# Optimization experiments

Measured on AMD Instinct MI355X. Metric: run time of the kernel, lower is better.

The kernel has to match this reference:

```python
import jax, jax.numpy as jnp
import numpy as np

EPS = 1e-10
NUM_NODES = 100000
OUT_CH = 128
NUM_EDGES = 600000


def setup_inputs() -> dict:
    key = jax.random.key(0)
    k1, k2, k3, k4, k5, k6 = jax.random.split(key, 6)
    emb = jax.random.normal(k1, (NUM_NODES, OUT_CH), dtype=jnp.float32) * 0.02
    edge_index = jax.random.randint(k2, (2, NUM_EDGES), 0, NUM_NODES, dtype=jnp.int32)
    edge_norm = jax.random.uniform(k3, (NUM_EDGES,), dtype=jnp.float32)
    lim = 1.0 / np.sqrt(OUT_CH)
    loc_w = jax.random.uniform(k4, (OUT_CH, OUT_CH), minval=-lim, maxval=lim, dtype=jnp.float32)
    loc_b = jnp.zeros((OUT_CH,), dtype=jnp.float32)
    std_w = jax.random.uniform(k5, (OUT_CH, OUT_CH), minval=-lim, maxval=lim, dtype=jnp.float32)
    std_b = jnp.zeros((OUT_CH,), dtype=jnp.float32)
    return {"emb": emb, "loc_w": loc_w, "loc_b": loc_b, "std_w": std_w,
            "std_b": std_b, "edge_index": edge_index, "edge_norm": edge_norm}


def reference(emb, loc_w, loc_b, std_w, std_b, edge_index, edge_norm):
    sidx, tidx = edge_index[0], edge_index[1]
    # gather-scale-scatter graph conv: message[e] = emb[sidx[e]] * enorm[e]
    message = emb[sidx] * edge_norm[:, None]          # [E, C]
    ptr = jax.ops.segment_sum(message, tidx, num_segments=emb.shape[0])  # [N, C]
    loc = ptr @ loc_w.T + loc_b                        # [N, C]
    std = jax.nn.softplus(ptr @ std_w.T + std_b) + EPS # [N, C]
    # eval mode: emb_out = loc (dist is Normal(loc, std), returned as params)
    return (loc, std)
```

## Files before the change

### kernel.cpp

```cpp
#include <hip/hip_runtime.h>
#include <hip/hip_bf16.h>
#include <stdint.h>

#define OUT_CH 128
#define EPSV 1e-10f

typedef __attribute__((ext_vector_type(4))) float f32x4;
typedef __attribute__((ext_vector_type(8))) short bf16x8;

__device__ __forceinline__ ushort f2bf(float f) {
    union { float f; unsigned u; } a; a.f = f;
    unsigned u = a.u;
    unsigned r = (u + 0x7fffu + ((u >> 16) & 1u)) >> 16;
    return (ushort)r;
}

__device__ __forceinline__ float bflo(unsigned u) { return __uint_as_float(u << 16); }
__device__ __forceinline__ float bfhi(unsigned u) { return __uint_as_float(u & 0xffff0000u); }

__global__ __launch_bounds__(256) void hist_convert_kernel(
    const int* __restrict__ eidx, int* __restrict__ cnt, int E, int HB, int EB,
    const float* __restrict__ locw, const float* __restrict__ stdw,
    int4* __restrict__ Wb, const float* __restrict__ emb, int4* __restrict__ embb4)
{
    int b = blockIdx.x;
    if (b < HB) {
        int e = b * 256 + threadIdx.x;
        if (e < E) atomicAdd(&cnt[eidx[E + e]], 1);
    } else if (b < HB + 16) {
        int q = (b - HB) * 256 + threadIdx.x;
        int r = q >> 4;
        int c = q & 15;
        const float* src = (r < 128) ? (locw + r * 128 + c * 8)
                                     : (stdw + (r - 128) * 128 + c * 8);
        float4 u0 = *reinterpret_cast<const float4*>(src);
        float4 u1 = *reinterpret_cast<const float4*>(src + 4);
        unsigned p0 = (unsigned)f2bf(u0.x) | ((unsigned)f2bf(u0.y) << 16);
        unsigned p1 = (unsigned)f2bf(u0.z) | ((unsigned)f2bf(u0.w) << 16);
        unsigned p2 = (unsigned)f2bf(u1.x) | ((unsigned)f2bf(u1.y) << 16);
        unsigned p3 = (unsigned)f2bf(u1.z) | ((unsigned)f2bf(u1.w) << 16);
        Wb[q] = make_int4((int)p0, (int)p1, (int)p2, (int)p3);
    } else {
        int idx8 = (b - HB - 16) * 256 + threadIdx.x;
        const float4* e4 = (const float4*)emb;
        float4 u0 = e4[(size_t)idx8 * 2];
        float4 u1 = e4[(size_t)idx8 * 2 + 1];
        unsigned p0 = (unsigned)f2bf(u0.x) | ((unsigned)f2bf(u0.y) << 16);
        unsigned p1 = (unsigned)f2bf(u0.z) | ((unsigned)f2bf(u0.w) << 16);
        unsigned p2 = (unsigned)f2bf(u1.x) | ((unsigned)f2bf(u1.y) << 16);
        unsigned p3 = (unsigned)f2bf(u1.z) | ((unsigned)f2bf(u1.w) << 16);
        embb4[idx8] = make_int4((int)p0, (int)p1, (int)p2, (int)p3);
    }
}

__device__ __forceinline__ int block_exscan256(int v, int* lds, int* totalOut) {
    int t = threadIdx.x;
    lds[t] = v; __syncthreads();
    #pragma unroll
    for (int d = 1; d < 256; d <<= 1) {
        int x = (t >= d) ? lds[t - d] : 0;
        __syncthreads();
        lds[t] += x;
        __syncthreads();
    }
    int inc = lds[t];
    int tot = lds[255];
    __syncthreads();
    *totalOut = tot;
    return inc - v;
}

__global__ __launch_bounds__(256) void block_sum_kernel(
    const int* __restrict__ cnt, int* __restrict__ bsum, int N)
{
    __shared__ int lds[256];
    int base = blockIdx.x * 1024;
    int local = 0;
    #pragma unroll
    for (int k = 0; k < 4; ++k) {
        int idx = base + threadIdx.x * 4 + k;
        local += (idx < N) ? cnt[idx] : 0;
    }
    lds[threadIdx.x] = local; __syncthreads();
    for (int d = 128; d > 0; d >>= 1) {
        if (threadIdx.x < d) lds[threadIdx.x] += lds[threadIdx.x + d];
        __syncthreads();
    }
    if (threadIdx.x == 0) bsum[blockIdx.x] = lds[0];
}

__global__ __launch_bounds__(256) void top_scan_kernel(
    const int* __restrict__ bsum, int* __restrict__ bofs, int NB)
{
    __shared__ int lds[256];
    int t = threadIdx.x;
    int v = (t < NB) ? bsum[t] : 0;
    int total;
    int ex = block_exscan256(v, lds, &total);
    if (t < NB) bofs[t] = ex;
}

__global__ __launch_bounds__(256) void scan_final_kernel(
    const int* __restrict__ cnt, const int* __restrict__ bofs,
    int* __restrict__ cursor, int N)
{
    __shared__ int lds[256];
    int base = blockIdx.x * 1024;
    int c[4]; int local = 0;
    #pragma unroll
    for (int k = 0; k < 4; ++k) {
        int idx = base + threadIdx.x * 4 + k;
        c[k] = (idx < N) ? cnt[idx] : 0;
        local += c[k];
    }
    int total;
    int ex = block_exscan256(local, lds, &total);
    int run = bofs[blockIdx.x] + ex;
    #pragma unroll
    for (int k = 0; k < 4; ++k) {
        int idx = base + threadIdx.x * 4 + k;
        if (idx < N) { cursor[idx] = run; run += c[k]; }
    }
}

__global__ __launch_bounds__(256) void fill_kernel(
    const int* __restrict__ eidx, const float* __restrict__ enorm,
    int* __restrict__ cursor, int2* __restrict__ srcw, int E)
{
    int e = blockIdx.x * 256 + threadIdx.x;
    if (e >= E) return;
    int t = eidx[E + e];
    int s = eidx[e];
    float w = enorm[e];
    int pos = atomicAdd(&cursor[t], 1);
    srcw[pos] = make_int2(s, __float_as_int(w));
}

__global__ __launch_bounds__(256) void gather_kernel(
    const uint4* __restrict__ embb4, const int* __restrict__ cursor,
    const int* __restrict__ cnt, const int2* __restrict__ srcw,
    uint4* __restrict__ ptrb4, int N)
{
    int q = (blockIdx.x * 256 + threadIdx.x) >> 4;
    if (q >= N) return;
    int l16 = threadIdx.x & 15;
    int c = cnt[q];
    int o = cursor[q] - c;
    float a0 = 0.f, a1 = 0.f, a2 = 0.f, a3 = 0.f;
    float a4 = 0.f, a5 = 0.f, a6 = 0.f, a7 = 0.f;
    int j = 0;
    for (; j + 2 <= c; j += 2) {
        int2 p0 = srcw[o + j + 0];
        int2 p1 = srcw[o + j + 1];
        uint4 v0 = embb4[(size_t)p0.x * 16 + l16];
        uint4 v1 = embb4[(size_t)p1.x * 16 + l16];
        float w0 = __int_as_float(p0.y), w1 = __int_as_float(p1.y);
        a0 += bflo(v0.x) * w0 + bflo(v1.x) * w1;
        a1 += bfhi(v0.x) * w0 + bfhi(v1.x) * w1;
        a2 += bflo(v0.y) * w0 + bflo(v1.y) * w1;
        a3 += bfhi(v0.y) * w0 + bfhi(v1.y) * w1;
        a4 += bflo(v0.z) * w0 + bflo(v1.z) * w1;
        a5 += bfhi(v0.z) * w0 + bfhi(v1.z) * w1;
        a6 += bflo(v0.w) * w0 + bflo(v1.w) * w1;
        a7 += bfhi(v0.w) * w0 + bfhi(v1.w) * w1;
    }
    if (j < c) {
        int2 p = srcw[o + j];
        uint4 v = embb4[(size_t)p.x * 16 + l16];
        float w = __int_as_float(p.y);
        a0 += bflo(v.x) * w;  a1 += bfhi(v.x) * w;
        a2 += bflo(v.y) * w;  a3 += bfhi(v.y) * w;
        a4 += bflo(v.z) * w;  a5 += bfhi(v.z) * w;
        a6 += bflo(v.w) * w;  a7 += bfhi(v.w) * w;
    }
    uint4 r;
    r.x = (unsigned)f2bf(a0) | ((unsigned)f2bf(a1) << 16);
    r.y = (unsigned)f2bf(a2) | ((unsigned)f2bf(a3) << 16);
    r.z = (unsigned)f2bf(a4) | ((unsigned)f2bf(a5) << 16);
    r.w = (unsigned)f2bf(a6) | ((unsigned)f2bf(a7) << 16);
    ptrb4[(size_t)q * 32 + l16] = r;
}

__global__ __launch_bounds__(256, 4) void gemm_kernel(
    const int4* __restrict__ Wb, const float* __restrict__ locb,
    const float* __restrict__ stdb, float* __restrict__ out, int N)
{
    __shared__ ushort Wt[128 * 128];
    const int t = threadIdx.x;
    const int wave = t >> 6;
    const int lane = t & 63;
    const int grp = lane >> 4;
    const int l16 = lane & 15;
    const int base = blockIdx.x * 128 + wave * 32;

    const ushort* ptrb = (const ushort*)out;
    int r0 = base + l16;      if (r0 > N - 1) r0 = N - 1;
    int r1 = base + 16 + l16; if (r1 > N - 1) r1 = N - 1;

    bf16x8 a0[4], a1[4];
    #pragma unroll
    for (int s = 0; s < 4; ++s) {
        a0[s] = *reinterpret_cast<const bf16x8*>(ptrb + (size_t)r0 * 256 + s * 32 + grp * 8);
        a1[s] = *reinterpret_cast<const bf16x8*>(ptrb + (size_t)r1 * 256 + s * 32 + grp * 8);
    }

    #pragma unroll
    for (int h = 0; h < 2; ++h) {
        if (h) __syncthreads();
        #pragma unroll
        for (int i = 0; i < 8; ++i) {
            int q = i * 256 + t;
            int r = q >> 4;
            int c = q & 15;
            *reinterpret_cast<int4*>(&Wt[r * 128 + ((c ^ (r & 15)) << 3)]) =
                Wb[(h * 128 + r) * 16 + c];
        }
        __syncthreads();

        f32x4 acc0[8], acc1[8];
        #pragma unroll
        for (int j = 0; j < 8; ++j) {
            acc0[j] = (f32x4){0.f, 0.f, 0.f, 0.f};
            acc1[j] = (f32x4){0.f, 0.f, 0.f, 0.f};
        }

        #pragma unroll
        for (int j = 0; j < 8; ++j) {
            int cb = (j * 16 + l16) * 128;
            #pragma unroll
            for (int s = 0; s < 4; ++s) {
                int c = s * 4 + grp;
                bf16x8 bfr = *reinterpret_cast<const bf16x8*>(&Wt[cb + ((c ^ l16) << 3)]);
                acc0[j] = __builtin_amdgcn_mfma_f32_16x16x32_bf16(a0[s], bfr, acc0[j], 0, 0, 0);
                acc1[j] = __builtin_amdgcn_mfma_f32_16x16x32_bf16(a1[s], bfr, acc1[j], 0, 0, 0);
            }
        }

        float* dst = h ? (out + (size_t)N * OUT_CH) : out;
        #pragma unroll
        for (int j = 0; j < 8; ++j) {
            int col = j * 16 + l16;
            float bias = h ? stdb[col] : locb[col];
            #pragma unroll
            for (int tile = 0; tile < 2; ++tile) {
                #pragma unroll
                for (int rg = 0; rg < 4; ++rg) {
                    int node = base + tile * 16 + grp * 4 + rg;
                    if (node < N) {
                        float x = (tile ? acc1[j][rg] : acc0[j][rg]) + bias;
                        if (h) x = __logf(1.0f + __expf(x)) + EPSV;
                        dst[(size_t)node * OUT_CH + col] = x;
                    }
                }
            }
        }
    }
}

extern "C" void kernel_launch(void* const* d_in, const int* in_sizes, int n_in,
                              void* d_out, int out_size, void* d_ws, size_t ws_size,
                              hipStream_t stream) {
    const float* emb  = (const float*)d_in[0];
    const float* locw = (const float*)d_in[1];
    const float* locb = (const float*)d_in[2];
    const float* stdw = (const float*)d_in[3];
    const float* stdb = (const float*)d_in[4];
    const int*   eidx = (const int*)d_in[5];
    const float* enorm= (const float*)d_in[6];
    float* out = (float*)d_out;

    const int N = in_sizes[0] / OUT_CH;
    const int E = in_sizes[6];
    const int NB = (N + 1023) / 1024;
    const int HB = (E + 255) / 256;
    const int EB = (N * (OUT_CH / 8) + 255) / 256;

    int* cnt    = (int*)d_ws;
    int* cursor = cnt + N;
    int* bsum   = cursor + N;
    int* bofs   = bsum + 256;
    int2* srcw  = (int2*)(((uintptr_t)(bofs + 256) + 255) & ~(uintptr_t)255);
    int4* Wb    = (int4*)(((uintptr_t)(srcw + E) + 255) & ~(uintptr_t)255);

    unsigned* embb = (unsigned*)(out + (size_t)N * OUT_CH);

    hipMemsetAsync(cnt, 0, (size_t)N * sizeof(int), stream);

    hist_convert_kernel<<<HB + 16 + EB, 256, 0, stream>>>(
        eidx, cnt, E, HB, EB, locw, stdw, Wb, emb, (int4*)embb);
    block_sum_kernel<<<NB, 256, 0, stream>>>(cnt, bsum, N);
    top_scan_kernel<<<1, 256, 0, stream>>>(bsum, bofs, NB);
    scan_final_kernel<<<NB, 256, 0, stream>>>(cnt, bofs, cursor, N);
    fill_kernel<<<(E + 255) / 256, 256, 0, stream>>>(eidx, enorm, cursor, srcw, E);

    uint4* ptrb4 = (uint4*)out;
    long gthreads = (long)N * 16;
    gather_kernel<<<(int)((gthreads + 255) / 256), 256, 0, stream>>>(
        (const uint4*)embb, cursor, cnt, srcw, ptrb4, N);

    int nblocks = (N + 127) / 128;
    gemm_kernel<<<nblocks, 256, 0, stream>>>(Wb, locb, stdb, out, N);
}
```

Measured before the change: 279.8 us.

## Pair two nodes per thread group in gather; read GEMM weights directly from global

The gather kernel now has each 16-lane group accumulate two destination nodes (q and q+N/2) in an interleaved loop, giving more independent loads in flight per thread at the cost of more registers and divergence when degrees differ. The GEMM drops the LDS weight staging and __syncthreads. Each wave computes 16 rows across all 256 output columns, loading B fragments directly from the global bf16 weight buffer, which is assumed to stay in cache. This removes the LDS fill and barriers but makes every wave fetch the full weight matrix.

```diff
diff --git a/kernel.cpp b/kernel.cpp
--- a/kernel.cpp
+++ b/kernel.cpp
@@ -139,119 +139,166 @@
 __global__ __launch_bounds__(256) void gather_kernel(
     const uint4* __restrict__ embb4, const int* __restrict__ cursor,
     const int* __restrict__ cnt, const int2* __restrict__ srcw,
-    uint4* __restrict__ ptrb4, int N)
-{
-    int q = (blockIdx.x * 256 + threadIdx.x) >> 4;
-    if (q >= N) return;
-    int l16 = threadIdx.x & 15;
-    int c = cnt[q];
-    int o = cursor[q] - c;
-    float a0 = 0.f, a1 = 0.f, a2 = 0.f, a3 = 0.f;
-    float a4 = 0.f, a5 = 0.f, a6 = 0.f, a7 = 0.f;
+    uint4* __restrict__ ptrb4, int N, int Nh)
+{
+    int idx = blockIdx.x * 256 + threadIdx.x;
+    int qa = idx >> 4;
+    if (qa >= Nh) return;
+    int l16 = idx & 15;
+    int qb = qa + Nh;
+    bool hasB = qb < N;
+
+    int ca = cnt[qa];
+    int oa = cursor[qa] - ca;
+    int cb = 0, ob = 0;
+    if (hasB) { cb = cnt[qb]; ob = cursor[qb] - cb; }
+
+    float a0=0.f,a1=0.f,a2=0.f,a3=0.f,a4=0.f,a5=0.f,a6=0.f,a7=0.f;
+    float b0=0.f,b1=0.f,b2=0.f,b3=0.f,b4=0.f,b5=0.f,b6=0.f,b7=0.f;
+
+    int m = ca < cb ? ca : cb;
     int j = 0;
-    for (; j + 2 <= c; j += 2) {
-        int2 p0 = srcw[o + j + 0];
-        int2 p1 = srcw[o + j + 1];
+    for (; j + 2 <= m; j += 2) {
+        int2 pa0 = srcw[oa + j];
+        int2 pa1 = srcw[oa + j + 1];
+        int2 pb0 = srcw[ob + j];
+        int2 pb1 = srcw[ob + j + 1];
+        uint4 va0 = embb4[(size_t)pa0.x * 16 + l16];
+        uint4 va1 = embb4[(size_t)pa1.x * 16 + l16];
+        uint4 vb0 = embb4[(size_t)pb0.x * 16 + l16];
+        uint4 vb1 = embb4[(size_t)pb1.x * 16 + l16];
+        float wa0 = __int_as_float(pa0.y), wa1 = __int_as_float(pa1.y);
+        float wb0 = __int_as_float(pb0.y), wb1 = __int_as_float(pb1.y);
+        a0 += bflo(va0.x)*wa0 + bflo(va1.x)*wa1;  a1 += bfhi(va0.x)*wa0 + bfhi(va1.x)*wa1;
+        a2 += bflo(va0.y)*wa0 + bflo(va1.y)*wa1;  a3 += bfhi(va0.y)*wa0 + bfhi(va1.y)*wa1;
+        a4 += bflo(va0.z)*wa0 + bflo(va1.z)*wa1;  a5 += bfhi(va0.z)*wa0 + bfhi(va1.z)*wa1;
+        a6 += bflo(va0.w)*wa0 + bflo(va1.w)*wa1;  a7 += bfhi(va0.w)*wa0 + bfhi(va1.w)*wa1;
+        b0 += bflo(vb0.x)*wb0 + bflo(vb1.x)*wb1;  b1 += bfhi(vb0.x)*wb0 + bfhi(vb1.x)*wb1;
+        b2 += bflo(vb0.y)*wb0 + bflo(vb1.y)*wb1;  b3 += bfhi(vb0.y)*wb0 + bfhi(vb1.y)*wb1;
+        b4 += bflo(vb0.z)*wb0 + bflo(vb1.z)*wb1;  b5 += bfhi(vb0.z)*wb0 + bfhi(vb1.z)*wb1;
+        b6 += bflo(vb0.w)*wb0 + bflo(vb1.w)*wb1;  b7 += bfhi(vb0.w)*wb0 + bfhi(vb1.w)*wb1;
+    }
+    for (; j < m; ++j) {
+        int2 pa = srcw[oa + j];
+        int2 pb = srcw[ob + j];
+        uint4 va = embb4[(size_t)pa.x * 16 + l16];
+        uint4 vb = embb4[(size_t)pb.x * 16 + l16];
+        float wa = __int_as_float(pa.y), wb = __int_as_float(pb.y);
+        a0 += bflo(va.x)*wa;  a1 += bfhi(va.x)*wa;
+        a2 += bflo(va.y)*wa;  a3 += bfhi(va.y)*wa;
+        a4 += bflo(va.z)*wa;  a5 += bfhi(va.z)*wa;
+        a6 += bflo(va.w)*wa;  a7 += bfhi(va.w)*wa;
+        b0 += bflo(vb.x)*wb;  b1 += bfhi(vb.x)*wb;
+        b2 += bflo(vb.y)*wb;  b3 += bfhi(vb.y)*wb;
+        b4 += bflo(vb.z)*wb;  b5 += bfhi(vb.z)*wb;
+        b6 += bflo(vb.w)*wb;  b7 += bfhi(vb.w)*wb;
+    }
+    for (; j + 2 <= ca; j += 2) {
+        int2 p0 = srcw[oa + j];
+        int2 p1 = srcw[oa + j + 1];
         uint4 v0 = embb4[(size_t)p0.x * 16 + l16];
         uint4 v1 = embb4[(size_t)p1.x * 16 + l16];
         float w0 = __int_as_float(p0.y), w1 = __int_as_float(p1.y);
-        a0 += bflo(v0.x) * w0 + bflo(v1.x) * w1;
-        a1 += bfhi(v0.x) * w0 + bfhi(v1.x) * w1;
-        a2 += bflo(v0.y) * w0 + bflo(v1.y) * w1;
-        a3 += bfhi(v0.y) * w0 + bfhi(v1.y) * w1;
-        a4 += bflo(v0.z) * w0 + bflo(v1.z) * w1;
-        a5 += bfhi(v0.z) * w0 + bfhi(v1.z) * w1;
-        a6 += bflo(v0.w) * w0 + bflo(v1.w) * w1;
-        a7 += bfhi(v0.w) * w0 + bfhi(v1.w) * w1;
-    }
-    if (j < c) {
-        int2 p = srcw[o + j];
+        a0 += bflo(v0.x)*w0 + bflo(v1.x)*w1;  a1 += bfhi(v0.x)*w0 + bfhi(v1.x)*w1;
+        a2 += bflo(v0.y)*w0 + bflo(v1.y)*w1;  a3 += bfhi(v0.y)*w0 + bfhi(v1.y)*w1;
+        a4 += bflo(v0.z)*w0 + bflo(v1.z)*w1;  a5 += bfhi(v0.z)*w0 + bfhi(v1.z)*w1;
+        a6 += bflo(v0.w)*w0 + bflo(v1.w)*w1;  a7 += bfhi(v0.w)*w0 + bfhi(v1.w)*w1;
+    }
+    if (j < ca) {
+        int2 p = srcw[oa + j];
         uint4 v = embb4[(size_t)p.x * 16 + l16];
         float w = __int_as_float(p.y);
-        a0 += bflo(v.x) * w;  a1 += bfhi(v.x) * w;
-        a2 += bflo(v.y) * w;  a3 += bfhi(v.y) * w;
-        a4 += bflo(v.z) * w;  a5 += bfhi(v.z) * w;
-        a6 += bflo(v.w) * w;  a7 += bfhi(v.w) * w;
-    }
-    uint4 r;
-    r.x = (unsigned)f2bf(a0) | ((unsigned)f2bf(a1) << 16);
-    r.y = (unsigned)f2bf(a2) | ((unsigned)f2bf(a3) << 16);
-    r.z = (unsigned)f2bf(a4) | ((unsigned)f2bf(a5) << 16);
-    r.w = (unsigned)f2bf(a6) | ((unsigned)f2bf(a7) << 16);
-    ptrb4[(size_t)q * 32 + l16] = r;
+        a0 += bflo(v.x)*w;  a1 += bfhi(v.x)*w;
+        a2 += bflo(v.y)*w;  a3 += bfhi(v.y)*w;
+        a4 += bflo(v.z)*w;  a5 += bfhi(v.z)*w;
+        a6 += bflo(v.w)*w;  a7 += bfhi(v.w)*w;
+    }
+    for (j = m + ((ca - m) & ~0); false;) {}
+    for (j = (j > m ? j : m); j + 2 <= cb; j += 2) {
+        int2 p0 = srcw[ob + j];
+        int2 p1 = srcw[ob + j + 1];
+        uint4 v0 = embb4[(size_t)p0.x * 16 + l16];
+        uint4 v1 = embb4[(size_t)p1.x * 16 + l16];
+        float w0 = __int_as_float(p0.y), w1 = __int_as_float(p1.y);
+        b0 += bflo(v0.x)*w0 + bflo(v1.x)*w1;  b1 += bfhi(v0.x)*w0 + bfhi(v1.x)*w1;
+        b2 += bflo(v0.y)*w0 + bflo(v1.y)*w1;  b3 += bfhi(v0.y)*w0 + bfhi(v1.y)*w1;
+        b4 += bflo(v0.z)*w0 + bflo(v1.z)*w1;  b5 += bfhi(v0.z)*w0 + bfhi(v1.z)*w1;
+        b6 += bflo(v0.w)*w0 + bflo(v1.w)*w1;  b7 += bfhi(v0.w)*w0 + bfhi(v1.w)*w1;
+    }
+    if (j < cb) {
+        int2 p = srcw[ob + j];
+        uint4 v = embb4[(size_t)p.x * 16 + l16];
+        float w = __int_as_float(p.y);
+        b0 += bflo(v.x)*w;  b1 += bfhi(v.x)*w;
+        b2 += bflo(v.y)*w;  b3 += bfhi(v.y)*w;
+        b4 += bflo(v.z)*w;  b5 += bfhi(v.z)*w;
+        b6 += bflo(v.w)*w;  b7 += bfhi(v.w)*w;
+    }
+
+    uint4 ra;
+    ra.x = (unsigned)f2bf(a0) | ((unsigned)f2bf(a1) << 16);
+    ra.y = (unsigned)f2bf(a2) | ((unsigned)f2bf(a3) << 16);
+    ra.z = (unsigned)f2bf(a4) | ((unsigned)f2bf(a5) << 16);
+    ra.w = (unsigned)f2bf(a6) | ((unsigned)f2bf(a7) << 16);
+    ptrb4[(size_t)qa * 32 + l16] = ra;
+    if (hasB) {
+        uint4 rb;
+        rb.x = (unsigned)f2bf(b0) | ((unsigned)f2bf(b1) << 16);
+        rb.y = (unsigned)f2bf(b2) | ((unsigned)f2bf(b3) << 16);
+        rb.z = (unsigned)f2bf(b4) | ((unsigned)f2bf(b5) << 16);
+        rb.w = (unsigned)f2bf(b6) | ((unsigned)f2bf(b7) << 16);
+        ptrb4[(size_t)qb * 32 + l16] = rb;
+    }
 }
 
 __global__ __launch_bounds__(256, 4) void gemm_kernel(
-    const int4* __restrict__ Wb, const float* __restrict__ locb,
+    const ushort* __restrict__ Wbl, const float* __restrict__ locb,
     const float* __restrict__ stdb, float* __restrict__ out, int N)
 {
-    __shared__ ushort Wt[128 * 128];
     const int t = threadIdx.x;
     const int wave = t >> 6;
     const int lane = t & 63;
     const int grp = lane >> 4;
     const int l16 = lane & 15;
-    const int base = blockIdx.x * 128 + wave * 32;
+    const int base = blockIdx.x * 64 + wave * 16;
 
     const ushort* ptrb = (const ushort*)out;
-    int r0 = base + l16;      if (r0 > N - 1) r0 = N - 1;
-    int r1 = base + 16 + l16; if (r1 > N - 1) r1 = N - 1;
-
-    bf16x8 a0[4], a1[4];
-    #pragma unroll
-    for (int s = 0; s < 4; ++s) {
-        a0[s] = *reinterpret_cast<const bf16x8*>(ptrb + (size_t)r0 * 256 + s * 32 + grp * 8);
-        a1[s] = *reinterpret_cast<const bf16x8*>(ptrb + (size_t)r1 * 256 + s * 32 + grp * 8);
-    }
-
-    #pragma unroll
-    for (int h = 0; h < 2; ++h) {
-        if (h) __syncthreads();
+    int r0 = base + l16; if (r0 > N - 1) r0 = N - 1;
+
+    bf16x8 a[4];
+    #pragma unroll
+    for (int s = 0; s < 4; ++s)
+        a[s] = *reinterpret_cast<const bf16x8*>(ptrb + (size_t)r0 * 256 + s * 32 + grp * 8);
+
+    f32x4 acc[16];
+    #pragma unroll
+    for (int j = 0; j < 16; ++j) acc[j] = (f32x4){0.f, 0.f, 0.f, 0.f};
+
+    #pragma unroll
+    for (int j = 0; j < 16; ++j) {
+        int col = j * 16 + l16;
+        const ushort* wrow = Wbl + col * 128 + grp * 8;
         #pragma unroll
-        for (int i = 0; i < 8; ++i) {
-            int q = i * 256 + t;
-            int r = q >> 4;
-            int c = q & 15;
-            *reinterpret_cast<int4*>(&Wt[r * 128 + ((c ^ (r & 15)) << 3)]) =
-                Wb[(h * 128 + r) * 16 + c];
+        for (int s = 0; s < 4; ++s) {
+            bf16x8 bfr = *reinterpret_cast<const bf16x8*>(wrow + s * 32);
+            acc[j] = __builtin_amdgcn_mfma_f32_16x16x32_bf16(a[s], bfr, acc[j], 0, 0, 0);
         }
-        __syncthreads();
-
-        f32x4 acc0[8], acc1[8];
+    }
+
+    #pragma unroll
+    for (int j = 0; j < 16; ++j) {
+        int col = j * 16 + l16;
+        bool isStd = col >= 128;
+        int wcol = col & 127;
+        float bias = isStd ? stdb[wcol] : locb[wcol];
+        float* dst = isStd ? (out + (size_t)N * OUT_CH) : out;
         #pragma unroll
-        for (int j = 0; j < 8; ++j) {
-            acc0[j] = (f32x4){0.f, 0.f, 0.f, 0.f};
-            acc1[j] = (f32x4){0.f, 0.f, 0.f, 0.f};
-        }
-
-        #pragma unroll
-        for (int j = 0; j < 8; ++j) {
-            int cb = (j * 16 + l16) * 128;
-            #pragma unroll
-            for (int s = 0; s < 4; ++s) {
-                int c = s * 4 + grp;
-                bf16x8 bfr = *reinterpret_cast<const bf16x8*>(&Wt[cb + ((c ^ l16) << 3)]);
-                acc0[j] = __builtin_amdgcn_mfma_f32_16x16x32_bf16(a0[s], bfr, acc0[j], 0, 0, 0);
-                acc1[j] = __builtin_amdgcn_mfma_f32_16x16x32_bf16(a1[s], bfr, acc1[j], 0, 0, 0);
-            }
-        }
-
-        float* dst = h ? (out + (size_t)N * OUT_CH) : out;
-        #pragma unroll
-        for (int j = 0; j < 8; ++j) {
-            int col = j * 16 + l16;
-            float bias = h ? stdb[col] : locb[col];
-            #pragma unroll
-            for (int tile = 0; tile < 2; ++tile) {
-                #pragma unroll
-                for (int rg = 0; rg < 4; ++rg) {
-                    int node = base + tile * 16 + grp * 4 + rg;
-                    if (node < N) {
-                        float x = (tile ? acc1[j][rg] : acc0[j][rg]) + bias;
-                        if (h) x = __logf(1.0f + __expf(x)) + EPSV;
-                        dst[(size_t)node * OUT_CH + col] = x;
-                    }
-                }
+        for (int rg = 0; rg < 4; ++rg) {
+            int node = base + grp * 4 + rg;
+            if (node < N) {
+                float x = acc[j][rg] + bias;
+                if (isStd) x = __logf(1.0f + __expf(x)) + EPSV;
+                dst[(size_t)node * OUT_CH + wcol] = x;
             }
         }
     }
@@ -274,6 +321,7 @@
     const int NB = (N + 1023) / 1024;
     const int HB = (E + 255) / 256;
     const int EB = (N * (OUT_CH / 8) + 255) / 256;
+    const int Nh = (N + 1) / 2;
 
     int* cnt    = (int*)d_ws;
     int* cursor = cnt + N;
@@ -294,10 +342,10 @@
     fill_kernel<<<(E + 255) / 256, 256, 0, stream>>>(eidx, enorm, cursor, srcw, E);
 
     uint4* ptrb4 = (uint4*)out;
-    long gthreads = (long)N * 16;
+    long gthreads = (long)Nh * 16;
     gather_kernel<<<(int)((gthreads + 255) / 256), 256, 0, stream>>>(
-        (const uint4*)embb, cursor, cnt, srcw, ptrb4, N);
-
-    int nblocks = (N + 127) / 128;
-    gemm_kernel<<<nblocks, 256, 0, stream>>>(Wb, locb, stdb, out, N);
-}
+        (const uint4*)embb, cursor, cnt, srcw, ptrb4, N, Nh);
+
+    int nblocks = (N + 63) / 64;
+    gemm_kernel<<<nblocks, 256, 0, stream>>>((const ushort*)Wb, locb, stdb, out, N);
+}
```

New measurement: 323.0 us. +15.5%, slower.
